# Kernel tuning notes

Measured on AMD Instinct MI355X. Metric: run time of the kernel, lower is better.

The kernel has to match this reference:

```python
import math
import jax, jax.numpy as jnp
import numpy as np

B, T, E = 2, 2048, 2048
NUM_HEADS = 16
H = NUM_HEADS // 2          # differential head pairs = 8
D = E // NUM_HEADS          # head_dim = 128
DEPTH = 12
LAMBDA_INIT = 0.8 - 0.6 * math.exp(-0.3 * DEPTH)
EPS = 1e-5


def setup_inputs() -> dict:
    key = jax.random.key(0)
    ks = jax.random.split(key, 10)
    sc = lambda k, shape, std: jax.random.normal(k, shape, dtype=jnp.float32) * std
    return {
        "x": jax.random.normal(ks[0], (B, T, E), dtype=jnp.float32),
        "Wq": sc(ks[1], (E, E), 0.02),   # [in, out]
        "Wk": sc(ks[2], (E, E), 0.02),   # n_rep == 1 -> k/v proj width = embed_dim
        "Wv": sc(ks[3], (E, E), 0.02),
        "Wo": sc(ks[4], (E, E), 0.02),
        "lambda_q1": sc(ks[5], (D,), 0.1),
        "lambda_k1": sc(ks[6], (D,), 0.1),
        "lambda_q2": sc(ks[7], (D,), 0.1),
        "lambda_k2": sc(ks[8], (D,), 0.1),
        "g": jnp.ones((2 * D,), dtype=jnp.float32),  # RMSNorm weight
    }


def _forward(x, Wq, Wk, Wv, Wo, lq1, lk1, lq2, lk2, g):
    Bz, Tl, _ = x.shape
    # projections; view(bsz, T, 2*H, D).reshape(bsz, T, H, 2, D): adjacent head
    # pairs become the two differential components.
    q = (x @ Wq).reshape(Bz, Tl, H, 2, D)
    k = (x @ Wk).reshape(Bz, Tl, H, 2, D)
    v = (x @ Wv).reshape(Bz, Tl, H, 2 * D)   # value width is 2*head_dim

    scale = D ** -0.5                         # SDPA default scaling
    causal = jnp.tril(jnp.ones((Tl, Tl), dtype=bool))  # is_causal=True

    def attend(qc, kc):
        # qc, kc: [B, T, H, D]
        s = jnp.einsum('bthd,bshd->bhts', qc, kc) * scale
        s = jnp.where(causal, s, -jnp.inf)
        a = jax.nn.softmax(s, axis=-1)
        return jnp.einsum('bhts,bshe->bthe', a, v)  # [B, T, H, 2D]

    # interleaved q/k + repeated v in the single SDPA == two attention maps on full V
    o1 = attend(q[..., 0, :], k[..., 0, :])
    o2 = attend(q[..., 1, :], k[..., 1, :])

    lam = jnp.exp(jnp.sum(lq1 * lk1)) - jnp.exp(jnp.sum(lq2 * lk2)) + LAMBDA_INIT
    o = o1 - lam * o2
    # RMSNorm over last dim (2*head_dim), eps=1e-5, learned weight g
    o = o * jax.lax.rsqrt(jnp.mean(o * o, axis=-1, keepdims=True) + EPS) * g
    o = o * (1.0 - LAMBDA_INIT)
    return o.reshape(Bz, Tl, E) @ Wo


def reference(x, Wq, Wk, Wv, Wo, lambda_q1, lambda_k1, lambda_q2, lambda_k2, g):
    return _forward(x, Wq, Wk, Wv, Wo, lambda_q1, lambda_k1, lambda_q2, lambda_k2, g)
```

## Files before the change

kernel.cpp:

```cpp
#include <hip/hip_runtime.h>
#include <stdint.h>
#include <math.h>


typedef unsigned short u16;
typedef short bf16x8 __attribute__((ext_vector_type(8)));
typedef float f32x4 __attribute__((ext_vector_type(4)));

typedef uint32_t __attribute__((address_space(1))) as1_u32;
typedef uint32_t __attribute__((address_space(3))) as3_u32;

#define LAMBDA_INIT 0.78360576653162453f

__device__ __forceinline__ u16 f2bf(float f) {
  uint32_t u = __float_as_uint(f);
  u += 0x7FFFu + ((u >> 16) & 1u);
  return (u16)(u >> 16);
}
__device__ __forceinline__ float bf2f(u16 v) {
  return __uint_as_float(((uint32_t)v) << 16);
}

__device__ __forceinline__ void async16(u16* lds, const u16* g) {
  __builtin_amdgcn_global_load_lds((const as1_u32*)(uintptr_t)g,
                                   (as3_u32*)(uint32_t)(uintptr_t)lds, 16, 0, 0);
}

__device__ __forceinline__ f32x4 mfma16(bf16x8 a, bf16x8 b, f32x4 c) {
  return __builtin_amdgcn_mfma_f32_16x16x32_bf16(a, b, c, 0, 0, 0);
}


__global__ void cast_x_kernel(const float* __restrict__ x, u16* __restrict__ xb, int n4) {
  int i = blockIdx.x * 256 + threadIdx.x;
  if (i < n4) {
    float4 v = ((const float4*)x)[i];
    ushort4 o;
    o.x = f2bf(v.x); o.y = f2bf(v.y); o.z = f2bf(v.z); o.w = f2bf(v.w);
    ((ushort4*)xb)[i] = o;
  }
}

__global__ void transpose_w4_kernel(const float* __restrict__ W0, const float* __restrict__ W1,
                                    const float* __restrict__ W2, const float* __restrict__ W3,
                                    u16* __restrict__ Wt4) {
  __shared__ float tile[32][33];
  int z = blockIdx.z;
  const float* W = (z == 0) ? W0 : (z == 1) ? W1 : (z == 2) ? W2 : W3;
  u16* Wt = Wt4 + (size_t)z * 4194304;
  int tx = threadIdx.x, ty = threadIdx.y;
  int c0 = blockIdx.x * 32, r0 = blockIdx.y * 32;
#pragma unroll
  for (int i = 0; i < 32; i += 8)
    tile[ty + i][tx] = W[(size_t)(r0 + ty + i) * 2048 + c0 + tx];
  __syncthreads();
#pragma unroll
  for (int i = 0; i < 32; i += 8)
    Wt[(size_t)(c0 + ty + i) * 2048 + r0 + tx] = f2bf(tile[tx][ty + i]);
}

__global__ void lam_kernel(const float* __restrict__ lq1, const float* __restrict__ lk1,
                           const float* __restrict__ lq2, const float* __restrict__ lk2,
                           float* __restrict__ out) {
  int L = threadIdx.x;
  float d1 = lq1[L] * lk1[L] + lq1[L + 64] * lk1[L + 64];
  float d2 = lq2[L] * lk2[L] + lq2[L + 64] * lk2[L + 64];
#pragma unroll
  for (int m = 1; m < 64; m <<= 1) {
    d1 += __shfl_xor(d1, m);
    d2 += __shfl_xor(d2, m);
  }
  if (L == 0) out[0] = __expf(d1) - __expf(d2) + LAMBDA_INIT;
}


__device__ __forceinline__ void stage256(const u16* base, int K, int k0, u16* lds, int t_) {
#pragma unroll
  for (int i = 0; i < 2; i++) {
    int s = t_ + i * 512;
    int row = s >> 2, gp = s & 3;
    int gs = gp ^ ((row >> 1) & 3);
    async16(&lds[s * 8], base + (size_t)row * K + k0 + gs * 8);
  }
}

__global__ __launch_bounds__(512, 2) void gemm256_kernel(const u16* __restrict__ A,
                                                         const u16* __restrict__ Bt,
                                                         u16* __restrict__ Cout,
                                                         int M, int N, int K) {
  __shared__ __attribute__((aligned(16))) u16 Ls[4][2][256 * 32];
  int t_ = threadIdx.x;
  int lane = t_ & 63, w = t_ >> 6;
  int lr = lane & 15, lq = lane >> 4;
  int m0 = blockIdx.y * 256, n0 = blockIdx.x * 256;
  int wm = (w >> 2) * 128, wn = (w & 3) * 64;
  const u16* Ab = A + (size_t)m0 * K;
  const u16* Bb = Bt + (size_t)n0 * K;
  int NT = K >> 5;
  f32x4 acc[8][4] = {};

#pragma unroll
  for (int p = 0; p < 3; p++) {
    stage256(Ab, K, p * 32, &Ls[p][0][0], t_);
    stage256(Bb, K, p * 32, &Ls[p][1][0], t_);
  }
  asm volatile("s_waitcnt vmcnt(8)" ::: "memory");
  __builtin_amdgcn_s_barrier();
  __builtin_amdgcn_sched_barrier(0);

#pragma unroll 1
  for (int t = 0; t < NT; t++) {
    int d = t & 3;
    const u16* As_ = &Ls[d][0][0];
    const u16* Bs_ = &Ls[d][1][0];
    bool stg = (t + 3 < NT);
    int k0n = (t + 3) * 32;
    int dn = (t + 3) & 3;

    bf16x8 b4[4], a0[4];
#pragma unroll
    for (int nf = 0; nf < 4; nf++) {
      int rb = wn + nf * 16 + lr;
      b4[nf] = *(const bf16x8*)&Bs_[rb * 32 + (lq ^ ((rb >> 1) & 3)) * 8];
    }
#pragma unroll
    for (int mf = 0; mf < 4; mf++) {
      int ra = wm + mf * 16 + lr;
      a0[mf] = *(const bf16x8*)&As_[ra * 32 + (lq ^ ((ra >> 1) & 3)) * 8];
    }
    if (stg) stage256(Ab, K, k0n, &Ls[dn][0][0], t_);
    __builtin_amdgcn_s_setprio(1);
#pragma unroll
    for (int mf = 0; mf < 4; mf++)
#pragma unroll
      for (int nf = 0; nf < 4; nf++)
        acc[mf][nf] = mfma16(a0[mf], b4[nf], acc[mf][nf]);
    __builtin_amdgcn_s_setprio(0);

    bf16x8 a1[4];
#pragma unroll
    for (int mf = 0; mf < 4; mf++) {
      int ra = wm + 64 + mf * 16 + lr;
      a1[mf] = *(const bf16x8*)&As_[ra * 32 + (lq ^ ((ra >> 1) & 3)) * 8];
    }
    if (stg) stage256(Bb, K, k0n, &Ls[dn][1][0], t_);
    __builtin_amdgcn_s_setprio(1);
#pragma unroll
    for (int mf = 0; mf < 4; mf++)
#pragma unroll
      for (int nf = 0; nf < 4; nf++)
        acc[4 + mf][nf] = mfma16(a1[mf], b4[nf], acc[4 + mf][nf]);
    __builtin_amdgcn_s_setprio(0);

    if (t < NT - 3)      asm volatile("s_waitcnt vmcnt(8)" ::: "memory");
    else if (t < NT - 2) asm volatile("s_waitcnt vmcnt(4)" ::: "memory");
    else                 asm volatile("s_waitcnt vmcnt(0)" ::: "memory");
    __builtin_amdgcn_s_barrier();
    __builtin_amdgcn_sched_barrier(0);
  }

#pragma unroll
  for (int mf = 0; mf < 8; mf++)
#pragma unroll
    for (int nf = 0; nf < 4; nf++)
#pragma unroll
      for (int r = 0; r < 4; r++) {
        int row = m0 + wm + mf * 16 + lq * 4 + r;
        int col = n0 + wn + nf * 16 + lr;
        Cout[(size_t)row * N + col] = f2bf(acc[mf][nf][r]);
      }
}

template <int OUT_BF16>
__global__ __launch_bounds__(256, 3) void gemm_bt_kernel(const u16* __restrict__ A,
                                                         const u16* __restrict__ Bt,
                                                         void* __restrict__ Cout,
                                                         int M, int N, int K) {
  __shared__ __attribute__((aligned(16))) u16 As[128 * 64];
  __shared__ __attribute__((aligned(16))) u16 Bs[128 * 64];
  int t = threadIdx.x;
  int lane = t & 63, w = t >> 6;
  int lr = lane & 15, lq = lane >> 4;
  int m0 = blockIdx.y * 128, n0 = blockIdx.x * 128;
  int wm = (w >> 1) * 64, wn = (w & 1) * 64;
  const u16* Ab = A + (size_t)m0 * K;
  const u16* Bb = Bt + (size_t)n0 * K;
  f32x4 acc[4][4] = {};

  for (int k0 = 0; k0 < K; k0 += 64) {
    __syncthreads();
#pragma unroll
    for (int i = 0; i < 4; i++) {
      int q = t + i * 256;
      int row = q >> 3, gp = q & 7;
      int gg = gp ^ (row & 7);
      async16(&As[q * 8], Ab + (size_t)row * K + k0 + gg * 8);
      async16(&Bs[q * 8], Bb + (size_t)row * K + k0 + gg * 8);
    }
    __syncthreads();
#pragma unroll
    for (int kk = 0; kk < 2; kk++) {
      bf16x8 a[4], b[4];
#pragma unroll
      for (int mi = 0; mi < 4; mi++) {
        int ra = wm + mi * 16 + lr;
        int rb = wn + mi * 16 + lr;
        a[mi] = *(const bf16x8*)&As[ra * 64 + ((kk * 4 + lq) ^ (ra & 7)) * 8];
        b[mi] = *(const bf16x8*)&Bs[rb * 64 + ((kk * 4 + lq) ^ (rb & 7)) * 8];
      }
#pragma unroll
      for (int mi = 0; mi < 4; mi++)
#pragma unroll
        for (int ni = 0; ni < 4; ni++)
          acc[mi][ni] = mfma16(a[mi], b[ni], acc[mi][ni]);
    }
  }
#pragma unroll
  for (int mi = 0; mi < 4; mi++) {
#pragma unroll
    for (int ni = 0; ni < 4; ni++) {
#pragma unroll
      for (int r = 0; r < 4; r++) {
        int row = m0 + wm + mi * 16 + lq * 4 + r;
        int col = n0 + wn + ni * 16 + lr;
        if (OUT_BF16)
          ((u16*)Cout)[(size_t)row * N + col] = f2bf(acc[mi][ni][r]);
        else
          ((float*)Cout)[(size_t)row * N + col] = acc[mi][ni][r];
      }
    }
  }
}


struct FlashCtx {
  const u16* Qbase;
  const u16* Kbase;
  const u16* Vbase;
  int t, w, lr, lq;
};

__device__ __forceinline__ void stage_k(const FlashCtx& cx, int jc, u16* Kn) {
#pragma unroll
  for (int i = 0; i < 4; i++) {
    int q = cx.t + i * 256;
    int row = q >> 4, gp = q & 15;
    int gg = (gp & 8) | ((gp & 7) ^ (row & 7));
    async16(&Kn[q * 8], cx.Kbase + (size_t)(jc + row) * 4096 + gg * 8);
  }
}

__device__ __forceinline__ void stage_v(const FlashCtx& cx, int jc, u16* Vs) {
#pragma unroll
  for (int i = 0; i < 8; i++) {
    int q = cx.t + i * 256;
    int e = q >> 3, gp = q & 7;
    int gg = gp ^ (e & 7);
    async16(&Vs[q * 8], cx.Vbase + (size_t)e * 4096 + jc + gg * 8);
  }
}

__global__ __launch_bounds__(256, 2) void flash_diff_kernel(const u16* __restrict__ QKb,
                                                            const u16* __restrict__ Vt,
                                                            u16* __restrict__ o12b) {
  __shared__ __attribute__((aligned(16))) u16 Ks0[64 * 128];
  __shared__ __attribute__((aligned(16))) u16 Ks1[64 * 128];
  __shared__ __attribute__((aligned(16))) u16 Vs[256 * 64];
  __shared__ __attribute__((aligned(16))) u16 Ps[4][16 * 88];

  int t = threadIdx.x;
  FlashCtx cx;
  cx.t = t; cx.w = t >> 6;
  cx.lr = t & 15; cx.lq = (t >> 4) & 3;

  int idx = blockIdx.x;
  int h = idx & 7;
  int slot = idx >> 3;
  int pairI = slot & 15;
  int hi2 = slot >> 4;
  int b = hi2 & 1, c = hi2 >> 1;

  cx.Qbase = QKb + (size_t)b * 2048 * 4096 + h * 256 + c * 128;
  cx.Kbase = cx.Qbase + 2048;
  cx.Vbase = Vt + (size_t)(h * 256) * 4096 + b * 2048;
  u16* Op = o12b + (size_t)c * (4096ull * 2048) + (size_t)b * 2048 * 2048 + h * 256;
  u16* PsW = Ps[cx.w];

  u16* Kc = Ks0;
  u16* Kn = Ks1;

  stage_k(cx, 0, Kc);

#pragma unroll 1
  for (int phase = 0; phase < 2; phase++) {
    int qi = phase ? (31 - pairI) : pairI;
    int q0 = qi * 64;
    int nst = qi + 1;

    bf16x8 qa[4];
#pragma unroll
    for (int ks = 0; ks < 4; ks++)
      qa[ks] = *(const bf16x8*)&cx.Qbase[(size_t)(q0 + cx.w * 16 + cx.lr) * 4096 +
                                         ks * 32 + cx.lq * 8];

    f32x4 acc[16] = {};
    f32x4 lacc = {};
    float m_ = -INFINITY;
    int rowmax = q0 + cx.w * 16 + 15;

#pragma unroll 1
    for (int j = 0; j < nst; j++) {
      int jc = j * 64;
      int njc = (j + 1 < nst) ? (j + 1) * 64 : (phase == 0 ? 0 : -1);

      __syncthreads();
      if (njc >= 0) stage_k(cx, njc, Kn);
      stage_v(cx, jc, Vs);

      bool act = (jc <= rowmax);
      if (act) {
        f32x4 sacc[4] = {};
#pragma unroll
        for (int ks = 0; ks < 4; ks++) {
#pragma unroll
          for (int ni = 0; ni < 4; ni++) {
            int row = ni * 16 + cx.lr;
            int gk = ks * 4 + cx.lq;
            int gp = (gk & 8) | ((gk & 7) ^ (row & 7));
            bf16x8 kb = *(const bf16x8*)&Kc[row * 128 + gp * 8];
            sacc[ni] = mfma16(qa[ks], kb, sacc[ni]);
          }
        }

        const float k2 = 0.12753257550036097f;
        float s2[4][4];
        bool diag = (jc + 63 > q0 + cx.w * 16);
#pragma unroll
        for (int ni = 0; ni < 4; ni++)
#pragma unroll
          for (int r = 0; r < 4; r++) {
            float v = sacc[ni][r] * k2;
            if (diag) {
              int colg = jc + ni * 16 + cx.lr;
              int rowg = q0 + cx.w * 16 + cx.lq * 4 + r;
              if (colg > rowg) v = -INFINITY;
            }
            s2[ni][r] = v;
          }

        float sm = fmaxf(
            fmaxf(fmaxf(fmaxf(s2[0][0], s2[0][1]), fmaxf(s2[0][2], s2[0][3])),
                  fmaxf(fmaxf(s2[1][0], s2[1][1]), fmaxf(s2[1][2], s2[1][3]))),
            fmaxf(fmaxf(fmaxf(s2[2][0], s2[2][1]), fmaxf(s2[2][2], s2[2][3])),
                  fmaxf(fmaxf(s2[3][0], s2[3][1]), fmaxf(s2[3][2], s2[3][3]))));
        float mo = m_;
        if (__any(sm > mo + 8.0f)) {
          float mv = sm;
          mv = fmaxf(mv, __shfl_xor(mv, 1));
          mv = fmaxf(mv, __shfl_xor(mv, 2));
          mv = fmaxf(mv, __shfl_xor(mv, 4));
          mv = fmaxf(mv, __shfl_xor(mv, 8));
          mv = fmaxf(mv, __shfl_xor(mv, 16));
          mv = fmaxf(mv, __shfl_xor(mv, 32));
          float mn = fmaxf(mo, mv);
          float a = __builtin_amdgcn_exp2f(mo - mn);
#pragma unroll
          for (int ei = 0; ei < 16; ei++)
#pragma unroll
            for (int r = 0; r < 4; r++) acc[ei][r] *= a;
#pragma unroll
          for (int r = 0; r < 4; r++) lacc[r] *= a;
          m_ = mn;
          mo = mn;
        }

#pragma unroll
        for (int ni = 0; ni < 4; ni++)
#pragma unroll
          for (int r = 0; r < 4; r++) {
            float p = __builtin_amdgcn_exp2f(s2[ni][r] - mo);
            PsW[(cx.lq * 4 + r) * 88 + ni * 16 + cx.lr] =
                (u16)(__float_as_uint(p) >> 16);
          }
      }

      __syncthreads();
      if (act) {
        const bf16x8 onesb = {0x3F80, 0x3F80, 0x3F80, 0x3F80,
                              0x3F80, 0x3F80, 0x3F80, 0x3F80};
        bf16x8 pa0 = *(const bf16x8*)&PsW[cx.lr * 88 + cx.lq * 8];
        bf16x8 pa1 = *(const bf16x8*)&PsW[cx.lr * 88 + 32 + cx.lq * 8];
        __builtin_amdgcn_s_setprio(1);
#pragma unroll
        for (int ei = 0; ei < 16; ei++) {
          int e = ei * 16 + cx.lr;
          int g0 = cx.lq ^ (e & 7);
          int g1 = g0 ^ 4;
          bf16x8 vb0 = *(const bf16x8*)&Vs[e * 64 + g0 * 8];
          bf16x8 vb1 = *(const bf16x8*)&Vs[e * 64 + g1 * 8];
          acc[ei] = mfma16(pa0, vb0, acc[ei]);
          acc[ei] = mfma16(pa1, vb1, acc[ei]);
        }
        lacc = mfma16(pa0, onesb, lacc);
        lacc = mfma16(pa1, onesb, lacc);
        __builtin_amdgcn_s_setprio(0);
      }

      u16* tmp = Kc; Kc = Kn; Kn = tmp;
    }

#pragma unroll
    for (int r = 0; r < 4; r++) {
      float inv = 1.0f / lacc[r];
      int row = q0 + cx.w * 16 + cx.lq * 4 + r;
#pragma unroll
      for (int ei = 0; ei < 16; ei++)
        Op[(size_t)row * 2048 + ei * 16 + cx.lr] = f2bf(acc[ei][r] * inv);
    }
  }
}

__global__ void combine_kernel(const u16* __restrict__ o12b, const float* __restrict__ lamp,
                               const float* __restrict__ g, u16* __restrict__ ob) {
  __shared__ float red[4];
  int t = threadIdx.x;
  int grp = blockIdx.x;
  size_t idx = (size_t)grp * 256 + t;
  const size_t comp = 4096ull * 2048;
  float lam = lamp[0];
  float v = bf2f(o12b[idx]) - lam * bf2f(o12b[idx + comp]);
  float ss = v * v;
  ss += __shfl_xor(ss, 1);
  ss += __shfl_xor(ss, 2);
  ss += __shfl_xor(ss, 4);
  ss += __shfl_xor(ss, 8);
  ss += __shfl_xor(ss, 16);
  ss += __shfl_xor(ss, 32);
  if ((t & 63) == 0) red[t >> 6] = ss;
  __syncthreads();
  float tot = red[0] + red[1] + red[2] + red[3];
  float scale = rsqrtf(tot * (1.0f / 256.0f) + 1e-5f) * (1.0f - LAMBDA_INIT);
  ob[(size_t)(grp >> 3) * 2048 + (grp & 7) * 256 + t] = f2bf(v * scale * g[t]);
}


extern "C" void kernel_launch(void* const* d_in, const int* in_sizes, int n_in,
                              void* d_out, int out_size, void* d_ws, size_t ws_size,
                              hipStream_t stream) {
  const float* x   = (const float*)d_in[0];
  const float* Wq  = (const float*)d_in[1];
  const float* Wk  = (const float*)d_in[2];
  const float* Wv  = (const float*)d_in[3];
  const float* Wo  = (const float*)d_in[4];
  const float* lq1 = (const float*)d_in[5];
  const float* lk1 = (const float*)d_in[6];
  const float* lq2 = (const float*)d_in[7];
  const float* lk2 = (const float*)d_in[8];
  const float* g   = (const float*)d_in[9];

  char* ws = (char*)d_ws;
  u16* xb    = (u16*)(ws);
  u16* Wtq   = (u16*)(ws + 16777216);
  u16* Wtv   = (u16*)(ws + 33554432);
  u16* Wto   = (u16*)(ws + 41943040);
  u16* QKb   = (u16*)(ws + 50331648);
  u16* Vt    = (u16*)(ws + 83886080);
  u16* o12b  = (u16*)(ws + 100663296);
  u16* ob    = (u16*)(ws + 134217728);
  float* lamp = (float*)(ws + 150994944);

  cast_x_kernel<<<8192, 256, 0, stream>>>(x, xb, 2097152);
  transpose_w4_kernel<<<dim3(64, 64, 4), dim3(32, 8), 0, stream>>>(Wq, Wk, Wv, Wo, Wtq);
  lam_kernel<<<1, 64, 0, stream>>>(lq1, lk1, lq2, lk2, lamp);

  gemm_bt_kernel<1><<<dim3(32, 16), 256, 0, stream>>>(Wtv, xb, Vt, 2048, 4096, 2048);
  gemm256_kernel<<<dim3(16, 16), 512, 0, stream>>>(xb, Wtq, QKb, 4096, 4096, 2048);

  flash_diff_kernel<<<512, 256, 0, stream>>>(QKb, Vt, o12b);
  combine_kernel<<<32768, 256, 0, stream>>>(o12b, lamp, g, ob);
  gemm_bt_kernel<0><<<dim3(16, 32), 256, 0, stream>>>(ob, Wto, (float*)d_out, 4096, 2048, 2048);
}
```

Measured before the change: 395.1 us.

## Fuse both differential attention maps and RMSNorm combine into one flash kernel

Merges the two per-component flash-attention blocks into a single 512-thread block in which waves 0-3 handle component 1 and waves 4-7 handle component 2. The blocks share K tiles holding both halves and a single V tile, so each V tile is loaded once instead of twice. The lambda combine and RMSNorm run inside the kernel through an LDS exchange, which removes the intermediate o12b round trip and the separate combine launch. K and V are now double-buffered with one barrier per iteration. The grid drops to 256 blocks, which may reduce occupancy and load balance, and LDS use per block grows substantially.

After: 380.6 us. 3.7% less time.

```diff
diff --git a/kernel.cpp b/kernel.cpp
--- a/kernel.cpp
+++ b/kernel.cpp
@@ -233,63 +233,66 @@
 }
 
 
-struct FlashCtx {
+struct F2Ctx {
   const u16* Qbase;
   const u16* Kbase;
   const u16* Vbase;
-  int t, w, lr, lq;
+  int t, w, wl, c, lr, lq;
 };
 
-__device__ __forceinline__ void stage_k(const FlashCtx& cx, int jc, u16* Kn) {
+__device__ __forceinline__ void stage_k2(const F2Ctx& cx, int jc, u16* Kb) {
 #pragma unroll
   for (int i = 0; i < 4; i++) {
-    int q = cx.t + i * 256;
-    int row = q >> 4, gp = q & 15;
-    int gg = (gp & 8) | ((gp & 7) ^ (row & 7));
-    async16(&Kn[q * 8], cx.Kbase + (size_t)(jc + row) * 4096 + gg * 8);
-  }
-}
-
-__device__ __forceinline__ void stage_v(const FlashCtx& cx, int jc, u16* Vs) {
-#pragma unroll
-  for (int i = 0; i < 8; i++) {
-    int q = cx.t + i * 256;
-    int e = q >> 3, gp = q & 7;
+    int s = cx.t + i * 512;
+    int row = s >> 5, gp = s & 31;
+    int gg = (gp & 24) | ((gp & 7) ^ (row & 7));
+    async16(&Kb[s * 8], cx.Kbase + (size_t)(jc + row) * 4096 + gg * 8);
+  }
+}
+
+__device__ __forceinline__ void stage_v2(const F2Ctx& cx, int jc, u16* Vb) {
+#pragma unroll
+  for (int i = 0; i < 4; i++) {
+    int s = cx.t + i * 512;
+    int e = s >> 3, gp = s & 7;
     int gg = gp ^ (e & 7);
-    async16(&Vs[q * 8], cx.Vbase + (size_t)e * 4096 + jc + gg * 8);
-  }
-}
-
-__global__ __launch_bounds__(256, 2) void flash_diff_kernel(const u16* __restrict__ QKb,
-                                                            const u16* __restrict__ Vt,
-                                                            u16* __restrict__ o12b) {
-  __shared__ __attribute__((aligned(16))) u16 Ks0[64 * 128];
-  __shared__ __attribute__((aligned(16))) u16 Ks1[64 * 128];
-  __shared__ __attribute__((aligned(16))) u16 Vs[256 * 64];
-  __shared__ __attribute__((aligned(16))) u16 Ps[4][16 * 88];
+    async16(&Vb[s * 8], cx.Vbase + (size_t)e * 4096 + jc + gg * 8);
+  }
+}
+
+__global__ __launch_bounds__(512, 2) void flash2_kernel(const u16* __restrict__ QKb,
+                                                        const u16* __restrict__ Vt,
+                                                        const float* __restrict__ lamp,
+                                                        const float* __restrict__ g,
+                                                        u16* __restrict__ ob) {
+  __shared__ __attribute__((aligned(16))) u16 Ks[2][64 * 256];
+  __shared__ __attribute__((aligned(16))) u16 Vs[2][256 * 64];
+  __shared__ __attribute__((aligned(16))) u16 Ps[8][16 * 88];
+  __shared__ float gsh[256];
 
   int t = threadIdx.x;
-  FlashCtx cx;
-  cx.t = t; cx.w = t >> 6;
+  F2Ctx cx;
+  cx.t = t; cx.w = t >> 6; cx.wl = cx.w & 3; cx.c = cx.w >> 2;
   cx.lr = t & 15; cx.lq = (t >> 4) & 3;
+
+  if (t < 256) gsh[t] = g[t];
 
   int idx = blockIdx.x;
   int h = idx & 7;
   int slot = idx >> 3;
   int pairI = slot & 15;
-  int hi2 = slot >> 4;
-  int b = hi2 & 1, c = hi2 >> 1;
-
-  cx.Qbase = QKb + (size_t)b * 2048 * 4096 + h * 256 + c * 128;
-  cx.Kbase = cx.Qbase + 2048;
+  int b = slot >> 4;
+
+  const u16* QKbh = QKb + (size_t)b * 2048 * 4096 + h * 256;
+  cx.Qbase = QKbh + cx.c * 128;
+  cx.Kbase = QKbh + 2048;
   cx.Vbase = Vt + (size_t)(h * 256) * 4096 + b * 2048;
-  u16* Op = o12b + (size_t)c * (4096ull * 2048) + (size_t)b * 2048 * 2048 + h * 256;
+  u16* obp = ob + (size_t)b * 2048 * 2048 + h * 256;
   u16* PsW = Ps[cx.w];
 
-  u16* Kc = Ks0;
-  u16* Kn = Ks1;
-
-  stage_k(cx, 0, Kc);
+  const float k2 = 0.12753257550036097f;
+  const bf16x8 onesb = {0x3F80, 0x3F80, 0x3F80, 0x3F80,
+                        0x3F80, 0x3F80, 0x3F80, 0x3F80};
 
 #pragma unroll 1
   for (int phase = 0; phase < 2; phase++) {
@@ -300,22 +303,27 @@
     bf16x8 qa[4];
 #pragma unroll
     for (int ks = 0; ks < 4; ks++)
-      qa[ks] = *(const bf16x8*)&cx.Qbase[(size_t)(q0 + cx.w * 16 + cx.lr) * 4096 +
+      qa[ks] = *(const bf16x8*)&cx.Qbase[(size_t)(q0 + cx.wl * 16 + cx.lr) * 4096 +
                                          ks * 32 + cx.lq * 8];
 
     f32x4 acc[16] = {};
     f32x4 lacc = {};
     float m_ = -INFINITY;
-    int rowmax = q0 + cx.w * 16 + 15;
+    int rowmax = q0 + cx.wl * 16 + 15;
+
+    stage_k2(cx, 0, Ks[0]);
+    stage_v2(cx, 0, Vs[0]);
+    __syncthreads();
 
 #pragma unroll 1
     for (int j = 0; j < nst; j++) {
       int jc = j * 64;
-      int njc = (j + 1 < nst) ? (j + 1) * 64 : (phase == 0 ? 0 : -1);
-
-      __syncthreads();
-      if (njc >= 0) stage_k(cx, njc, Kn);
-      stage_v(cx, jc, Vs);
+      if (j + 1 < nst) {
+        stage_k2(cx, jc + 64, Ks[(j + 1) & 1]);
+        stage_v2(cx, jc + 64, Vs[(j + 1) & 1]);
+      }
+      const u16* Kc = Ks[j & 1];
+      const u16* Vc = Vs[j & 1];
 
       bool act = (jc <= rowmax);
       if (act) {
@@ -325,16 +333,15 @@
 #pragma unroll
           for (int ni = 0; ni < 4; ni++) {
             int row = ni * 16 + cx.lr;
-            int gk = ks * 4 + cx.lq;
-            int gp = (gk & 8) | ((gk & 7) ^ (row & 7));
-            bf16x8 kb = *(const bf16x8*)&Kc[row * 128 + gp * 8];
+            int gk = cx.c * 16 + ks * 4 + cx.lq;
+            int gp = (gk & 24) | ((gk & 7) ^ (row & 7));
+            bf16x8 kb = *(const bf16x8*)&Kc[row * 256 + gp * 8];
             sacc[ni] = mfma16(qa[ks], kb, sacc[ni]);
           }
         }
 
-        const float k2 = 0.12753257550036097f;
         float s2[4][4];
-        bool diag = (jc + 63 > q0 + cx.w * 16);
+        bool diag = (jc + 63 > q0 + cx.wl * 16);
 #pragma unroll
         for (int ni = 0; ni < 4; ni++)
 #pragma unroll
@@ -342,7 +349,7 @@
             float v = sacc[ni][r] * k2;
             if (diag) {
               int colg = jc + ni * 16 + cx.lr;
-              int rowg = q0 + cx.w * 16 + cx.lq * 4 + r;
+              int rowg = q0 + cx.wl * 16 + cx.lq * 4 + r;
               if (colg > rowg) v = -INFINITY;
             }
             s2[ni][r] = v;
@@ -382,12 +389,7 @@
             PsW[(cx.lq * 4 + r) * 88 + ni * 16 + cx.lr] =
                 (u16)(__float_as_uint(p) >> 16);
           }
-      }
-
-      __syncthreads();
-      if (act) {
-        const bf16x8 onesb = {0x3F80, 0x3F80, 0x3F80, 0x3F80,
-                              0x3F80, 0x3F80, 0x3F80, 0x3F80};
+
         bf16x8 pa0 = *(const bf16x8*)&PsW[cx.lr * 88 + cx.lq * 8];
         bf16x8 pa1 = *(const bf16x8*)&PsW[cx.lr * 88 + 32 + cx.lq * 8];
         __builtin_amdgcn_s_setprio(1);
@@ -396,8 +398,8 @@
           int e = ei * 16 + cx.lr;
           int g0 = cx.lq ^ (e & 7);
           int g1 = g0 ^ 4;
-          bf16x8 vb0 = *(const bf16x8*)&Vs[e * 64 + g0 * 8];
-          bf16x8 vb1 = *(const bf16x8*)&Vs[e * 64 + g1 * 8];
+          bf16x8 vb0 = *(const bf16x8*)&Vc[e * 64 + g0 * 8];
+          bf16x8 vb1 = *(const bf16x8*)&Vc[e * 64 + g1 * 8];
           acc[ei] = mfma16(pa0, vb0, acc[ei]);
           acc[ei] = mfma16(pa1, vb1, acc[ei]);
         }
@@ -406,41 +408,50 @@
         __builtin_amdgcn_s_setprio(0);
       }
 
-      u16* tmp = Kc; Kc = Kn; Kn = tmp;
-    }
-
-#pragma unroll
-    for (int r = 0; r < 4; r++) {
-      float inv = 1.0f / lacc[r];
-      int row = q0 + cx.w * 16 + cx.lq * 4 + r;
-#pragma unroll
-      for (int ei = 0; ei < 16; ei++)
-        Op[(size_t)row * 2048 + ei * 16 + cx.lr] = f2bf(acc[ei][r] * inv);
-    }
-  }
-}
-
-__global__ void combine_kernel(const u16* __restrict__ o12b, const float* __restrict__ lamp,
-                               const float* __restrict__ g, u16* __restrict__ ob) {
-  __shared__ float red[4];
-  int t = threadIdx.x;
-  int grp = blockIdx.x;
-  size_t idx = (size_t)grp * 256 + t;
-  const size_t comp = 4096ull * 2048;
-  float lam = lamp[0];
-  float v = bf2f(o12b[idx]) - lam * bf2f(o12b[idx + comp]);
-  float ss = v * v;
-  ss += __shfl_xor(ss, 1);
-  ss += __shfl_xor(ss, 2);
-  ss += __shfl_xor(ss, 4);
-  ss += __shfl_xor(ss, 8);
-  ss += __shfl_xor(ss, 16);
-  ss += __shfl_xor(ss, 32);
-  if ((t & 63) == 0) red[t >> 6] = ss;
-  __syncthreads();
-  float tot = red[0] + red[1] + red[2] + red[3];
-  float scale = rsqrtf(tot * (1.0f / 256.0f) + 1e-5f) * (1.0f - LAMBDA_INIT);
-  ob[(size_t)(grp >> 3) * 2048 + (grp & 7) * 256 + t] = f2bf(v * scale * g[t]);
+      __syncthreads();
+    }
+
+    u16* Os = (u16*)&Ks[0][0];
+    if (cx.c == 1) {
+#pragma unroll
+      for (int r = 0; r < 4; r++) {
+        float inv = 1.0f / lacc[r];
+        int rowL = cx.wl * 16 + cx.lq * 4 + r;
+#pragma unroll
+        for (int ei = 0; ei < 16; ei++)
+          Os[rowL * 256 + ei * 16 + cx.lr] = f2bf(acc[ei][r] * inv);
+      }
+    }
+    __syncthreads();
+    if (cx.c == 0) {
+      float lam = lamp[0];
+#pragma unroll
+      for (int r = 0; r < 4; r++) {
+        float inv = 1.0f / lacc[r];
+        int rowL = cx.wl * 16 + cx.lq * 4 + r;
+        float vv[16];
+        float ss = 0.0f;
+#pragma unroll
+        for (int ei = 0; ei < 16; ei++) {
+          float o1 = acc[ei][r] * inv;
+          float o2 = bf2f(Os[rowL * 256 + ei * 16 + cx.lr]);
+          float v = o1 - lam * o2;
+          vv[ei] = v;
+          ss += v * v;
+        }
+        ss += __shfl_xor(ss, 1);
+        ss += __shfl_xor(ss, 2);
+        ss += __shfl_xor(ss, 4);
+        ss += __shfl_xor(ss, 8);
+        float scale = rsqrtf(ss * (1.0f / 256.0f) + 1e-5f) * (1.0f - LAMBDA_INIT);
+        size_t rowG = (size_t)(q0 + rowL) * 2048;
+#pragma unroll
+        for (int ei = 0; ei < 16; ei++)
+          obp[rowG + ei * 16 + cx.lr] = f2bf(vv[ei] * scale * gsh[ei * 16 + cx.lr]);
+      }
+    }
+    __syncthreads();
+  }
 }
 
 
@@ -465,7 +476,6 @@
   u16* Wto   = (u16*)(ws + 41943040);
   u16* QKb   = (u16*)(ws + 50331648);
   u16* Vt    = (u16*)(ws + 83886080);
-  u16* o12b  = (u16*)(ws + 100663296);
   u16* ob    = (u16*)(ws + 134217728);
   float* lamp = (float*)(ws + 150994944);
 
@@ -476,7 +486,6 @@
   gemm_bt_kernel<1><<<dim3(32, 16), 256, 0, stream>>>(Wtv, xb, Vt, 2048, 4096, 2048);
   gemm256_kernel<<<dim3(16, 16), 512, 0, stream>>>(xb, Wtq, QKb, 4096, 4096, 2048);
 
-  flash_diff_kernel<<<512, 256, 0, stream>>>(QKb, Vt, o12b);
-  combine_kernel<<<32768, 256, 0, stream>>>(o12b, lamp, g, ob);
+  flash2_kernel<<<256, 512, 0, stream>>>(QKb, Vt, lamp, g, ob);
   gemm_bt_kernel<0><<<dim3(16, 32), 256, 0, stream>>>(ob, Wto, (float*)d_out, 4096, 2048, 2048);
 }
```
